# Kernel optimization log

Hardware: AMD Instinct MI355X
Metric: run time of the kernel (lower is better)

The kernel has to match this reference:

```python
import jax, jax.numpy as jnp
import numpy as np


def _dwconv(x, w, b, pad):
    # x: [B, C, H, W]; w: [C, 1, kh, kw]; depthwise via feature_group_count=C
    y = jax.lax.conv_general_dilated(
        x, w, window_strides=(1, 1), padding=pad,
        dimension_numbers=("NCHW", "OIHW", "NCHW"),
        feature_group_count=x.shape[1])
    return y + b[None, :, None, None]


def setup_inputs() -> dict:
    key = jax.random.key(0)
    ks = jax.random.split(key, 16)
    dim, B, H, W = 128, 32, 64, 64
    def w_init(k, shape):
        fan_in = int(np.prod(shape[1:]))
        return jax.random.normal(k, shape, jnp.float32) * (1.0 / np.sqrt(fan_in))
    return {
        "x": jax.random.normal(ks[0], (B, dim, H, W), jnp.float32),
        "w0": w_init(ks[1], (dim, 1, 5, 5)),   "b0": jax.random.normal(ks[2], (dim,), jnp.float32) * 0.01,
        "w0_1": w_init(ks[3], (dim, 1, 1, 7)), "b0_1": jax.random.normal(ks[4], (dim,), jnp.float32) * 0.01,
        "w0_2": w_init(ks[5], (dim, 1, 7, 1)), "b0_2": jax.random.normal(ks[6], (dim,), jnp.float32) * 0.01,
        "w1_1": w_init(ks[7], (dim, 1, 1, 15)), "b1_1": jax.random.normal(ks[8], (dim,), jnp.float32) * 0.01,
        "w1_2": w_init(ks[9], (dim, 1, 15, 1)), "b1_2": jax.random.normal(ks[10], (dim,), jnp.float32) * 0.01,
        "w2_1": w_init(ks[11], (dim, 1, 1, 31)), "b2_1": jax.random.normal(ks[12], (dim,), jnp.float32) * 0.01,
        "w2_2": w_init(ks[13], (dim, 1, 31, 1)), "b2_2": jax.random.normal(ks[14], (dim,), jnp.float32) * 0.01,
    }


def reference(x, w0, b0, w0_1, b0_1, w0_2, b0_2, w1_1, b1_1, w1_2, b1_2, w2_1, b2_1, w2_2, b2_2):
    attn = _dwconv(x, w0, b0, ((2, 2), (2, 2)))
    attn_0 = _dwconv(attn, w0_1, b0_1, ((0, 0), (3, 3)))
    attn_0 = _dwconv(attn_0, w0_2, b0_2, ((3, 3), (0, 0)))
    attn_1 = _dwconv(attn, w1_1, b1_1, ((0, 0), (7, 7)))
    attn_1 = _dwconv(attn_1, w1_2, b1_2, ((7, 7), (0, 0)))
    attn_2 = _dwconv(attn, w2_1, b2_1, ((0, 0), (15, 15)))
    attn_2 = _dwconv(attn_2, w2_2, b2_2, ((15, 15), (0, 0)))
    return jnp.concatenate((x, attn, attn_0, attn_1, attn_2), axis=1)
```

## Files before the change

kernel.cpp:

```cpp
#include <hip/hip_runtime.h>

#define TPB 256

#define ATT_STRIDE 100
#define ATT_SIZE   (64 * 100)
#define XS_STRIDE  76
#define TS_STRIDE  68
#define UNI_SIZE   (96 * 68)

template <int K>
__device__ __forceinline__ void h_pass(const int tid, const float* __restrict__ att,
                                       float* __restrict__ uni, const float* __restrict__ wl,
                                       const int whoff, const int bhoff) {
    constexpr int T = 2 * K + 1;
    constexpr int S0 = (16 - K) & ~3;
    constexpr int L4 = ((16 - K - S0) + 16 + 2 * K + 3) / 4;
    const int i = tid >> 2;
    const int j0 = (tid & 3) << 4;
    float wr[T];
#pragma unroll
    for (int d = 0; d < T; ++d) wr[d] = wl[whoff + d];
    const float bh = wl[bhoff];
    float raw[4 * L4];
#pragma unroll
    for (int k = 0; k < L4; ++k)
        *(float4*)&raw[4 * k] = *(const float4*)&att[i * ATT_STRIDE + j0 + S0 + 4 * k];
    float acc[16];
#pragma unroll
    for (int jj = 0; jj < 16; ++jj) acc[jj] = bh;
#pragma unroll
    for (int d = 0; d < T; ++d) {
        const float w = wr[d];
#pragma unroll
        for (int jj = 0; jj < 16; ++jj) acc[jj] += raw[jj + d + 1] * w;
    }
#pragma unroll
    for (int q = 0; q < 4; ++q)
        *(float4*)&uni[(i + 16) * TS_STRIDE + j0 + 4 * q] =
            make_float4(acc[4 * q], acc[4 * q + 1], acc[4 * q + 2], acc[4 * q + 3]);
}

template <int K>
__device__ __forceinline__ void v_pass(const int tid, const float* __restrict__ uni,
                                       const float* __restrict__ wl,
                                       const int wvoff, const int bvoff,
                                       float* __restrict__ outblk) {
    constexpr int T = 2 * K + 1;
    constexpr int W = 16 + 2 * K;
    const int j = tid & 63;
    const int i0 = (tid >> 6) << 4;
    float wr[T];
#pragma unroll
    for (int d = 0; d < T; ++d) wr[d] = wl[wvoff + d];
    const float bv = wl[bvoff];
    float win[W];
#pragma unroll
    for (int d = 0; d < W; ++d)
        win[d] = uni[(i0 - K + d + 16) * TS_STRIDE + j];
    float acc[16];
#pragma unroll
    for (int ii = 0; ii < 16; ++ii) acc[ii] = bv;
#pragma unroll
    for (int d = 0; d < T; ++d) {
        const float w = wr[d];
#pragma unroll
        for (int ii = 0; ii < 16; ++ii) acc[ii] += win[ii + d] * w;
    }
    float* op = outblk + i0 * 64 + j;
#pragma unroll
    for (int ii = 0; ii < 16; ++ii) op[ii * 64] = acc[ii];
}

__global__ __launch_bounds__(TPB, 3)
void lka_fused_kernel(const float* __restrict__ x,
                      const float* __restrict__ w0,  const float* __restrict__ b0,
                      const float* __restrict__ w01, const float* __restrict__ b01,
                      const float* __restrict__ w02, const float* __restrict__ b02,
                      const float* __restrict__ w11, const float* __restrict__ b11,
                      const float* __restrict__ w12, const float* __restrict__ b12,
                      const float* __restrict__ w21, const float* __restrict__ b21,
                      const float* __restrict__ w22, const float* __restrict__ b22,
                      float* __restrict__ out) {
    __shared__ __align__(16) float att[ATT_SIZE];
    __shared__ __align__(16) float uni[UNI_SIZE];
    __shared__ __align__(16) float wl[144];

    const int tid = threadIdx.x;
    const int plane = blockIdx.x;
    const int b = plane >> 7;
    const int c = plane & 127;

    const float* xp = x + (size_t)plane * 4096;
    float* outb = out + ((size_t)b * 640 + (size_t)c) * 4096;

    {
        const float4 z4 = make_float4(0.f, 0.f, 0.f, 0.f);
        float4* a4 = (float4*)att;
#pragma unroll
        for (int k = tid; k < ATT_SIZE / 4; k += TPB) a4[k] = z4;
        float4* u4 = (float4*)uni;
#pragma unroll
        for (int k = tid; k < UNI_SIZE / 4; k += TPB) u4[k] = z4;
    }
    if (tid < 25)        wl[tid] = w0 [c * 25 + tid];
    else if (tid < 32)   wl[tid] = w01[c * 7  + tid - 25];
    else if (tid < 39)   wl[tid] = w02[c * 7  + tid - 32];
    else if (tid < 54)   wl[tid] = w11[c * 15 + tid - 39];
    else if (tid < 69)   wl[tid] = w12[c * 15 + tid - 54];
    else if (tid < 100)  wl[tid] = w21[c * 31 + tid - 69];
    else if (tid < 131)  wl[tid] = w22[c * 31 + tid - 100];
    else if (tid == 131) wl[131] = b0 [c];
    else if (tid == 132) wl[132] = b01[c];
    else if (tid == 133) wl[133] = b02[c];
    else if (tid == 134) wl[134] = b11[c];
    else if (tid == 135) wl[135] = b12[c];
    else if (tid == 136) wl[136] = b21[c];
    else if (tid == 137) wl[137] = b22[c];
    __syncthreads();

    {
        const float4* x4 = (const float4*)xp;
        float4* o4 = (float4*)outb;
#pragma unroll
        for (int s = 0; s < 4; ++s) {
            const int idx = tid + s * TPB;
            const float4 v = x4[idx];
            o4[idx] = v;
            const int r = idx >> 4;
            const int c0 = (idx & 15) << 2;
            *(float4*)&uni[(r + 2) * XS_STRIDE + c0 + 4] = v;
        }
    }
    __syncthreads();

    {
        const int i = tid >> 2;
        const int j0 = (tid & 3) << 4;
        float wr[25];
#pragma unroll
        for (int d = 0; d < 25; ++d) wr[d] = wl[d];
        const float bias = wl[131];
        float acc[16];
#pragma unroll
        for (int jj = 0; jj < 16; ++jj) acc[jj] = bias;
#pragma unroll
        for (int a = 0; a < 5; ++a) {
            float raw[24];
#pragma unroll
            for (int k = 0; k < 6; ++k)
                *(float4*)&raw[4 * k] = *(const float4*)&uni[(i + a) * XS_STRIDE + j0 + 4 * k];
#pragma unroll
            for (int bb = 0; bb < 5; ++bb) {
                const float w = wr[a * 5 + bb];
#pragma unroll
                for (int jj = 0; jj < 16; ++jj) acc[jj] += raw[jj + bb + 2] * w;
            }
        }
        float* op = outb + (size_t)1 * 128 * 4096 + i * 64 + j0;
#pragma unroll
        for (int q = 0; q < 4; ++q) {
            const float4 v = make_float4(acc[4 * q], acc[4 * q + 1], acc[4 * q + 2], acc[4 * q + 3]);
            ((float4*)op)[q] = v;
            *(float4*)&att[i * ATT_STRIDE + j0 + 16 + 4 * q] = v;
        }
    }
    __syncthreads();

    {
        const float4 z4 = make_float4(0.f, 0.f, 0.f, 0.f);
        float4* u4 = (float4*)uni;
#pragma unroll
        for (int k = tid; k < 272; k += TPB) u4[k] = z4;
#pragma unroll
        for (int k = tid; k < 272; k += TPB) u4[1360 + k] = z4;
    }
    h_pass<3>(tid, att, uni, wl, 25, 132);
    __syncthreads();
    v_pass<3>(tid, uni, wl, 32, 133, outb + (size_t)2 * 128 * 4096);
    __syncthreads();

    h_pass<7>(tid, att, uni, wl, 39, 134);
    __syncthreads();
    v_pass<7>(tid, uni, wl, 54, 135, outb + (size_t)3 * 128 * 4096);
    __syncthreads();

    h_pass<15>(tid, att, uni, wl, 69, 136);
    __syncthreads();
    v_pass<15>(tid, uni, wl, 100, 137, outb + (size_t)4 * 128 * 4096);
}

extern "C" void kernel_launch(void* const* d_in, const int* in_sizes, int n_in,
                              void* d_out, int out_size, void* d_ws, size_t ws_size,
                              hipStream_t stream) {
    const float* x   = (const float*)d_in[0];
    const float* w0  = (const float*)d_in[1];
    const float* b0  = (const float*)d_in[2];
    const float* w01 = (const float*)d_in[3];
    const float* b01 = (const float*)d_in[4];
    const float* w02 = (const float*)d_in[5];
    const float* b02 = (const float*)d_in[6];
    const float* w11 = (const float*)d_in[7];
    const float* b11 = (const float*)d_in[8];
    const float* w12 = (const float*)d_in[9];
    const float* b12 = (const float*)d_in[10];
    const float* w21 = (const float*)d_in[11];
    const float* b21 = (const float*)d_in[12];
    const float* w22 = (const float*)d_in[13];
    const float* b22 = (const float*)d_in[14];
    float* out = (float*)d_out;

    lka_fused_kernel<<<dim3(4096), dim3(TPB), 0, stream>>>(
        x, w0, b0, w01, b01, w02, b02, w11, b11, w12, b12, w21, b21, w22, b22, out);
}
```

Baseline: 422.9 us.

## Split fused LKA kernel into conv5 kernel and parallel per-branch kernel

The single fused kernel, which ran the three strip-conv branches one after another per plane, is replaced by two launches. The first computes the 5x5 depthwise conv and copies x. The second runs each branch as its own block (grid y=3), reading attn back from global output with predicated boundary handling instead of zero-padded shared buffers. This cuts shared memory per block and raises the occupancy target to gain parallelism. The cost is a second launch and a global re-read of attn, which is likely to hit in L2.

```diff
diff --git a/kernel.cpp b/kernel.cpp
--- a/kernel.cpp
+++ b/kernel.cpp
@@ -2,122 +2,31 @@
 
 #define TPB 256
 
-#define ATT_STRIDE 100
-#define ATT_SIZE   (64 * 100)
-#define XS_STRIDE  76
-#define TS_STRIDE  68
-#define UNI_SIZE   (96 * 68)
+#define XS_STRIDE 76
+#define XS_SIZE   (68 * 76)
 
-template <int K>
-__device__ __forceinline__ void h_pass(const int tid, const float* __restrict__ att,
-                                       float* __restrict__ uni, const float* __restrict__ wl,
-                                       const int whoff, const int bhoff) {
-    constexpr int T = 2 * K + 1;
-    constexpr int S0 = (16 - K) & ~3;
-    constexpr int L4 = ((16 - K - S0) + 16 + 2 * K + 3) / 4;
-    const int i = tid >> 2;
-    const int j0 = (tid & 3) << 4;
-    float wr[T];
-#pragma unroll
-    for (int d = 0; d < T; ++d) wr[d] = wl[whoff + d];
-    const float bh = wl[bhoff];
-    float raw[4 * L4];
-#pragma unroll
-    for (int k = 0; k < L4; ++k)
-        *(float4*)&raw[4 * k] = *(const float4*)&att[i * ATT_STRIDE + j0 + S0 + 4 * k];
-    float acc[16];
-#pragma unroll
-    for (int jj = 0; jj < 16; ++jj) acc[jj] = bh;
-#pragma unroll
-    for (int d = 0; d < T; ++d) {
-        const float w = wr[d];
-#pragma unroll
-        for (int jj = 0; jj < 16; ++jj) acc[jj] += raw[jj + d + 1] * w;
-    }
-#pragma unroll
-    for (int q = 0; q < 4; ++q)
-        *(float4*)&uni[(i + 16) * TS_STRIDE + j0 + 4 * q] =
-            make_float4(acc[4 * q], acc[4 * q + 1], acc[4 * q + 2], acc[4 * q + 3]);
-}
+#define TS_STRIDE 68
+#define TS_SIZE   (64 * 68)
 
-template <int K>
-__device__ __forceinline__ void v_pass(const int tid, const float* __restrict__ uni,
-                                       const float* __restrict__ wl,
-                                       const int wvoff, const int bvoff,
-                                       float* __restrict__ outblk) {
-    constexpr int T = 2 * K + 1;
-    constexpr int W = 16 + 2 * K;
-    const int j = tid & 63;
-    const int i0 = (tid >> 6) << 4;
-    float wr[T];
-#pragma unroll
-    for (int d = 0; d < T; ++d) wr[d] = wl[wvoff + d];
-    const float bv = wl[bvoff];
-    float win[W];
-#pragma unroll
-    for (int d = 0; d < W; ++d)
-        win[d] = uni[(i0 - K + d + 16) * TS_STRIDE + j];
-    float acc[16];
-#pragma unroll
-    for (int ii = 0; ii < 16; ++ii) acc[ii] = bv;
-#pragma unroll
-    for (int d = 0; d < T; ++d) {
-        const float w = wr[d];
-#pragma unroll
-        for (int ii = 0; ii < 16; ++ii) acc[ii] += win[ii + d] * w;
-    }
-    float* op = outblk + i0 * 64 + j;
-#pragma unroll
-    for (int ii = 0; ii < 16; ++ii) op[ii * 64] = acc[ii];
-}
-
-__global__ __launch_bounds__(TPB, 3)
-void lka_fused_kernel(const float* __restrict__ x,
-                      const float* __restrict__ w0,  const float* __restrict__ b0,
-                      const float* __restrict__ w01, const float* __restrict__ b01,
-                      const float* __restrict__ w02, const float* __restrict__ b02,
-                      const float* __restrict__ w11, const float* __restrict__ b11,
-                      const float* __restrict__ w12, const float* __restrict__ b12,
-                      const float* __restrict__ w21, const float* __restrict__ b21,
-                      const float* __restrict__ w22, const float* __restrict__ b22,
+__global__ __launch_bounds__(TPB, 4)
+void lka_conv5_kernel(const float* __restrict__ x,
+                      const float* __restrict__ w0, const float* __restrict__ b0,
                       float* __restrict__ out) {
-    __shared__ __align__(16) float att[ATT_SIZE];
-    __shared__ __align__(16) float uni[UNI_SIZE];
-    __shared__ __align__(16) float wl[144];
-
+    __shared__ __align__(16) float xs[XS_SIZE];
     const int tid = threadIdx.x;
     const int plane = blockIdx.x;
     const int b = plane >> 7;
     const int c = plane & 127;
-
     const float* xp = x + (size_t)plane * 4096;
     float* outb = out + ((size_t)b * 640 + (size_t)c) * 4096;
 
     {
         const float4 z4 = make_float4(0.f, 0.f, 0.f, 0.f);
-        float4* a4 = (float4*)att;
+        float4* u4 = (float4*)xs;
 #pragma unroll
-        for (int k = tid; k < ATT_SIZE / 4; k += TPB) a4[k] = z4;
-        float4* u4 = (float4*)uni;
-#pragma unroll
-        for (int k = tid; k < UNI_SIZE / 4; k += TPB) u4[k] = z4;
+        for (int k = tid; k < XS_SIZE / 4; k += TPB) u4[k] = z4;
     }
-    if (tid < 25)        wl[tid] = w0 [c * 25 + tid];
-    else if (tid < 32)   wl[tid] = w01[c * 7  + tid - 25];
-    else if (tid < 39)   wl[tid] = w02[c * 7  + tid - 32];
-    else if (tid < 54)   wl[tid] = w11[c * 15 + tid - 39];
-    else if (tid < 69)   wl[tid] = w12[c * 15 + tid - 54];
-    else if (tid < 100)  wl[tid] = w21[c * 31 + tid - 69];
-    else if (tid < 131)  wl[tid] = w22[c * 31 + tid - 100];
-    else if (tid == 131) wl[131] = b0 [c];
-    else if (tid == 132) wl[132] = b01[c];
-    else if (tid == 133) wl[133] = b02[c];
-    else if (tid == 134) wl[134] = b11[c];
-    else if (tid == 135) wl[135] = b12[c];
-    else if (tid == 136) wl[136] = b21[c];
-    else if (tid == 137) wl[137] = b22[c];
     __syncthreads();
-
     {
         const float4* x4 = (const float4*)xp;
         float4* o4 = (float4*)outb;
@@ -128,18 +37,15 @@
             o4[idx] = v;
             const int r = idx >> 4;
             const int c0 = (idx & 15) << 2;
-            *(float4*)&uni[(r + 2) * XS_STRIDE + c0 + 4] = v;
+            *(float4*)&xs[(r + 2) * XS_STRIDE + c0 + 4] = v;
         }
     }
     __syncthreads();
-
     {
         const int i = tid >> 2;
         const int j0 = (tid & 3) << 4;
-        float wr[25];
-#pragma unroll
-        for (int d = 0; d < 25; ++d) wr[d] = wl[d];
-        const float bias = wl[131];
+        const float* wp = w0 + c * 25;
+        const float bias = b0[c];
         float acc[16];
 #pragma unroll
         for (int jj = 0; jj < 16; ++jj) acc[jj] = bias;
@@ -148,45 +54,117 @@
             float raw[24];
 #pragma unroll
             for (int k = 0; k < 6; ++k)
-                *(float4*)&raw[4 * k] = *(const float4*)&uni[(i + a) * XS_STRIDE + j0 + 4 * k];
+                *(float4*)&raw[4 * k] = *(const float4*)&xs[(i + a) * XS_STRIDE + j0 + 4 * k];
 #pragma unroll
             for (int bb = 0; bb < 5; ++bb) {
-                const float w = wr[a * 5 + bb];
+                const float w = wp[a * 5 + bb];
 #pragma unroll
                 for (int jj = 0; jj < 16; ++jj) acc[jj] += raw[jj + bb + 2] * w;
             }
         }
-        float* op = outb + (size_t)1 * 128 * 4096 + i * 64 + j0;
+        float* op = outb + (size_t)128 * 4096 + i * 64 + j0;
 #pragma unroll
-        for (int q = 0; q < 4; ++q) {
-            const float4 v = make_float4(acc[4 * q], acc[4 * q + 1], acc[4 * q + 2], acc[4 * q + 3]);
-            ((float4*)op)[q] = v;
-            *(float4*)&att[i * ATT_STRIDE + j0 + 16 + 4 * q] = v;
+        for (int q = 0; q < 4; ++q)
+            ((float4*)op)[q] = make_float4(acc[4 * q], acc[4 * q + 1],
+                                           acc[4 * q + 2], acc[4 * q + 3]);
+    }
+}
+
+template <int K>
+__device__ __forceinline__ void branch_pass(
+    const int tid, const int c,
+    const float* __restrict__ att,
+    const float* __restrict__ wh, const float* __restrict__ bh,
+    const float* __restrict__ wv, const float* __restrict__ bv,
+    float* __restrict__ op0, float* __restrict__ t) {
+    constexpr int T = 2 * K + 1;
+    constexpr int KA = K + 1;
+    constexpr int NW4 = (KA + 16 + K + 3) / 4;
+    constexpr int W = 16 + 2 * K;
+
+    {
+        const int i = tid >> 2;
+        const int j0 = (tid & 3) << 4;
+        const float* arow = att + i * 64;
+        float raw[4 * NW4];
+#pragma unroll
+        for (int q = 0; q < NW4; ++q) {
+            const int col0 = j0 - KA + 4 * q;
+            const bool ok = (unsigned)col0 < 61u;
+            const float4 v = *(const float4*)&arow[ok ? col0 : 0];
+            raw[4 * q + 0] = ok ? v.x : 0.f;
+            raw[4 * q + 1] = ok ? v.y : 0.f;
+            raw[4 * q + 2] = ok ? v.z : 0.f;
+            raw[4 * q + 3] = ok ? v.w : 0.f;
         }
+        const float* whp = wh + c * T;
+        const float bias = bh[c];
+        float acc[16];
+#pragma unroll
+        for (int jj = 0; jj < 16; ++jj) acc[jj] = bias;
+#pragma unroll
+        for (int d = 0; d < T; ++d) {
+            const float w = whp[d];
+#pragma unroll
+            for (int jj = 0; jj < 16; ++jj) acc[jj] += raw[jj + d + 1] * w;
+        }
+#pragma unroll
+        for (int q = 0; q < 4; ++q)
+            *(float4*)&t[i * TS_STRIDE + j0 + 4 * q] =
+                make_float4(acc[4 * q], acc[4 * q + 1], acc[4 * q + 2], acc[4 * q + 3]);
     }
     __syncthreads();
 
     {
-        const float4 z4 = make_float4(0.f, 0.f, 0.f, 0.f);
-        float4* u4 = (float4*)uni;
+        const int j = tid & 63;
+        const int i0 = (tid >> 6) << 4;
+        float win[W];
 #pragma unroll
-        for (int k = tid; k < 272; k += TPB) u4[k] = z4;
+        for (int dd = 0; dd < W; ++dd) {
+            const int r = i0 - K + dd;
+            const int rc = min(max(r, 0), 63);
+            const float v = t[rc * TS_STRIDE + j];
+            win[dd] = (r == rc) ? v : 0.f;
+        }
+        const float* wvp = wv + c * T;
+        const float bias = bv[c];
+        float acc[16];
 #pragma unroll
-        for (int k = tid; k < 272; k += TPB) u4[1360 + k] = z4;
+        for (int ii = 0; ii < 16; ++ii) acc[ii] = bias;
+#pragma unroll
+        for (int d = 0; d < T; ++d) {
+            const float w = wvp[d];
+#pragma unroll
+            for (int ii = 0; ii < 16; ++ii) acc[ii] += win[ii + d] * w;
+        }
+        float* op = op0 + i0 * 64 + j;
+#pragma unroll
+        for (int ii = 0; ii < 16; ++ii) op[ii * 64] = acc[ii];
     }
-    h_pass<3>(tid, att, uni, wl, 25, 132);
-    __syncthreads();
-    v_pass<3>(tid, uni, wl, 32, 133, outb + (size_t)2 * 128 * 4096);
-    __syncthreads();
+}
 
-    h_pass<7>(tid, att, uni, wl, 39, 134);
-    __syncthreads();
-    v_pass<7>(tid, uni, wl, 54, 135, outb + (size_t)3 * 128 * 4096);
-    __syncthreads();
+__global__ __launch_bounds__(TPB, 4)
+void lka_branch_kernel(float* out,
+                       const float* __restrict__ w01, const float* __restrict__ b01,
+                       const float* __restrict__ w02, const float* __restrict__ b02,
+                       const float* __restrict__ w11, const float* __restrict__ b11,
+                       const float* __restrict__ w12, const float* __restrict__ b12,
+                       const float* __restrict__ w21, const float* __restrict__ b21,
+                       const float* __restrict__ w22, const float* __restrict__ b22) {
+    __shared__ __align__(16) float t[TS_SIZE];
+    const int tid = threadIdx.x;
+    const int plane = blockIdx.x;
+    const int b = plane >> 7;
+    const int c = plane & 127;
+    const float* att = out + ((size_t)b * 640 + 128 + (size_t)c) * 4096;
+    float* op = out + ((size_t)b * 640 + (size_t)(2 + blockIdx.y) * 128 + (size_t)c) * 4096;
 
-    h_pass<15>(tid, att, uni, wl, 69, 136);
-    __syncthreads();
-    v_pass<15>(tid, uni, wl, 100, 137, outb + (size_t)4 * 128 * 4096);
+    if (blockIdx.y == 0)
+        branch_pass<3>(tid, c, att, w01, b01, w02, b02, op, t);
+    else if (blockIdx.y == 1)
+        branch_pass<7>(tid, c, att, w11, b11, w12, b12, op, t);
+    else
+        branch_pass<15>(tid, c, att, w21, b21, w22, b22, op, t);
 }
 
 extern "C" void kernel_launch(void* const* d_in, const int* in_sizes, int n_in,
@@ -209,6 +187,7 @@
     const float* b22 = (const float*)d_in[14];
     float* out = (float*)d_out;
 
-    lka_fused_kernel<<<dim3(4096), dim3(TPB), 0, stream>>>(
-        x, w0, b0, w01, b01, w02, b02, w11, b11, w12, b12, w21, b21, w22, b22, out);
+    lka_conv5_kernel<<<dim3(4096), dim3(TPB), 0, stream>>>(x, w0, b0, out);
+    lka_branch_kernel<<<dim3(4096, 3), dim3(TPB), 0, stream>>>(
+        out, w01, b01, w02, b02, w11, b11, w12, b12, w21, b21, w22, b22);
 }
```

New measurement: 450.4 us. 1.06x slower.
